# Kernel tuning notes

Measured on AMD Instinct MI355X. Metric: run time of the kernel, lower is better.

Reference implementation:

```python
import jax, jax.numpy as jnp
import numpy as np

DIM = 192
NUM_HEADS = 6
HEAD_DIM = DIM // NUM_HEADS
SCALE = HEAD_DIM ** -0.5


def setup_inputs() -> dict:
    key = jax.random.key(0)
    ks = jax.random.split(key, 4)
    B_, N, C = 4096, 64, DIM  # num_windows*B, Wh*Ww, dim
    nW = 64
    w_std = 0.02  # trunc-normal-ish init scale to keep logits sane
    x = jax.random.normal(ks[0], (B_, N, C), dtype=jnp.float32)
    mask = jnp.zeros((nW, N, N), dtype=jnp.float32)  # 0/-inf shift mask; zeros here
    qkv_w = jax.random.normal(ks[1], (3 * C, C), dtype=jnp.float32) * w_std
    qkv_b = jnp.zeros((3 * C,), dtype=jnp.float32)
    proj_w = jax.random.normal(ks[2], (C, C), dtype=jnp.float32) * w_std
    proj_b = jnp.zeros((C,), dtype=jnp.float32)
    return {"x": x, "mask": mask, "qkv_w": qkv_w, "qkv_b": qkv_b,
            "proj_w": proj_w, "proj_b": proj_b}


def reference(x, mask, qkv_w, qkv_b, proj_w, proj_b):
    B_, N, C = x.shape
    H, hd = NUM_HEADS, HEAD_DIM
    # qkv projection: torch Linear is x @ W.T + b
    qkv = x @ qkv_w.T + qkv_b                       # [B_, N, 3C]
    qkv = qkv.reshape(B_, N, 3, H, hd)
    qkv = jnp.transpose(qkv, (2, 0, 3, 1, 4))       # [3, B_, H, N, hd]
    q, k, v = qkv[0], qkv[1], qkv[2]
    attn = jnp.einsum('bhnd,bhmd->bhnm', q * SCALE, k)  # [B_, H, N, N]
    nW = mask.shape[0]
    attn = attn.reshape(B_ // nW, nW, H, N, N) + mask[None, :, None, :, :]
    attn = jax.nn.softmax(attn.reshape(B_, H, N, N), axis=-1)
    out = jnp.einsum('bhnm,bhmd->bnhd', attn, v).reshape(B_, N, C)
    out = out @ proj_w.T + proj_b
    return out
```

## Files before the change

kernel.cpp:

```cpp
#include <hip/hip_runtime.h>
#include <stdint.h>
#include <stddef.h>

#define NWIN   64
#define NTOK   64
#define CDIM   192
#define NHEAD  6
#define HDIM   32
constexpr float SCALE = 0.17677669529663687f;

typedef float   f32x4  __attribute__((ext_vector_type(4)));
typedef float   fvec4  __attribute__((ext_vector_type(4)));
typedef __bf16  bfx8   __attribute__((ext_vector_type(8)));
typedef __bf16  bfx4   __attribute__((ext_vector_type(4)));

static __device__ __forceinline__ bfx8 pack8(fvec4 a, fvec4 b) {
  bfx8 r;
  r[0] = (__bf16)a[0]; r[1] = (__bf16)a[1]; r[2] = (__bf16)a[2]; r[3] = (__bf16)a[3];
  r[4] = (__bf16)b[0]; r[5] = (__bf16)b[1]; r[6] = (__bf16)b[2]; r[7] = (__bf16)b[3];
  return r;
}

#define LDS_BYTES 130048

__global__ void __launch_bounds__(512, 1)
wattn_fused(const float* __restrict__ x, const float* __restrict__ mask,
            const float* __restrict__ qkv_w, const float* __restrict__ qkv_b,
            const float* __restrict__ proj_w, const float* __restrict__ proj_b,
            float* __restrict__ out)
{
  extern __shared__ char smem[];
  __bf16* qk = (__bf16*)(smem);
  __bf16* vT = (__bf16*)(smem + 50176);
  float*  pf = (float*)(smem + 77824);
  __bf16* pb = (__bf16*)(smem + 95232);
  __bf16* xb = (__bf16*)(smem + 104448);
  __bf16* ao = xb;

  const int b    = blockIdx.x;
  const int tid  = threadIdx.x;
  const int wv   = tid >> 6;
  const int lane = tid & 63;
  const int r16  = lane & 15;
  const int q4   = lane >> 4;

  {
    const float* xg = x + (size_t)b * (NTOK * CDIM);
#pragma unroll
    for (int it = 0; it < 6; ++it) {
      int i   = tid + it * 512;
      int row = i / 48;
      int col = (i % 48) * 4;
      fvec4 v = *(const fvec4*)(xg + i * 4);
      bfx4 p; p[0] = (__bf16)v[0]; p[1] = (__bf16)v[1];
              p[2] = (__bf16)v[2]; p[3] = (__bf16)v[3];
      *(bfx4*)(xb + row * 200 + col) = p;
    }
  }
  __syncthreads();

  {
    f32x4 acc[5][4];
#pragma unroll
    for (int cl = 0; cl < 5; ++cl)
#pragma unroll
      for (int rt = 0; rt < 4; ++rt) acc[cl][rt] = (f32x4){0.f, 0.f, 0.f, 0.f};

    for (int k = 0; k < 6; ++k) {
      bfx8 af[4];
#pragma unroll
      for (int rt = 0; rt < 4; ++rt)
        af[rt] = *(const bfx8*)(xb + (rt * 16 + r16) * 200 + k * 32 + q4 * 8);
#pragma unroll
      for (int cl = 0; cl < 5; ++cl) {
        int ct = wv + cl * 8;
        if (ct < 36) {
          const float* wp = qkv_w + (size_t)(ct * 16 + r16) * 192 + k * 32 + q4 * 8;
          bfx8 bf = pack8(*(const fvec4*)wp, *(const fvec4*)(wp + 4));
#pragma unroll
          for (int rt = 0; rt < 4; ++rt)
            acc[cl][rt] = __builtin_amdgcn_mfma_f32_16x16x32_bf16(
                af[rt], bf, acc[cl][rt], 0, 0, 0);
        }
      }
    }
#pragma unroll
    for (int cl = 0; cl < 5; ++cl) {
      int ct = wv + cl * 8;
      if (ct < 36) {
        float bias = qkv_b[ct * 16 + r16];
        if (ct < 24) {
#pragma unroll
          for (int rt = 0; rt < 4; ++rt) {
#pragma unroll
            for (int r = 0; r < 4; ++r)
              qk[(rt * 16 + q4 * 4 + r) * 392 + ct * 16 + r16] =
                  (__bf16)(acc[cl][rt][r] + bias);
          }
        } else {
          int h = (ct - 24) >> 1;
          int d = ((ct - 24) & 1) * 16 + r16;
#pragma unroll
          for (int rt = 0; rt < 4; ++rt) {
            bfx4 p;
#pragma unroll
            for (int r = 0; r < 4; ++r) p[r] = (__bf16)(acc[cl][rt][r] + bias);
            *(bfx4*)(vT + (h * 32 + d) * 72 + rt * 16 + q4 * 4) = p;
          }
        }
      }
    }
  }
  __syncthreads();

  const int wmask = b & (NWIN - 1);
  for (int h = 0; h < 6; ++h) {
    {
      int nt = wv >> 1;
      bfx8 qf = *(const bfx8*)(qk + (nt * 16 + r16) * 392 + h * 32 + q4 * 8);
      f32x4 z = (f32x4){0.f, 0.f, 0.f, 0.f};
#pragma unroll
      for (int j = 0; j < 2; ++j) {
        int mt = (wv & 1) * 2 + j;
        bfx8 kf = *(const bfx8*)(qk + (mt * 16 + r16) * 392 + 192 + h * 32 + q4 * 8);
        f32x4 s = __builtin_amdgcn_mfma_f32_16x16x32_bf16(qf, kf, z, 0, 0, 0);
#pragma unroll
        for (int r = 0; r < 4; ++r)
          pf[(nt * 16 + q4 * 4 + r) * 68 + mt * 16 + r16] = s[r];
      }
    }
    __syncthreads();
    {
      int n  = tid >> 3;
      int s8 = (tid & 7) * 8;
      const float* mrow = mask + ((size_t)wmask * 64 + n) * 64 + s8;
      fvec4 m0 = *(const fvec4*)(mrow);
      fvec4 m1 = *(const fvec4*)(mrow + 4);
      float v[8];
#pragma unroll
      for (int i = 0; i < 4; ++i) v[i]     = pf[n * 68 + s8 + i]     * SCALE + m0[i];
#pragma unroll
      for (int i = 0; i < 4; ++i) v[4 + i] = pf[n * 68 + s8 + 4 + i] * SCALE + m1[i];
      float mx = v[0];
#pragma unroll
      for (int i = 1; i < 8; ++i) mx = fmaxf(mx, v[i]);
      mx = fmaxf(mx, __shfl_xor(mx, 1));
      mx = fmaxf(mx, __shfl_xor(mx, 2));
      mx = fmaxf(mx, __shfl_xor(mx, 4));
      float sum = 0.f;
#pragma unroll
      for (int i = 0; i < 8; ++i) { v[i] = __expf(v[i] - mx); sum += v[i]; }
      sum += __shfl_xor(sum, 1);
      sum += __shfl_xor(sum, 2);
      sum += __shfl_xor(sum, 4);
      float inv = 1.f / sum;
      bfx8 p;
#pragma unroll
      for (int i = 0; i < 8; ++i) p[i] = (__bf16)(v[i] * inv);
      *(bfx8*)(pb + n * 72 + s8) = p;
    }
    __syncthreads();
    {
      int nt = wv >> 1, dt = wv & 1;
      f32x4 acc = (f32x4){0.f, 0.f, 0.f, 0.f};
#pragma unroll
      for (int kk = 0; kk < 2; ++kk) {
        bfx8 pa = *(const bfx8*)(pb + (nt * 16 + r16) * 72 + kk * 32 + q4 * 8);
        bfx8 vb = *(const bfx8*)(vT + (h * 32 + dt * 16 + r16) * 72 + kk * 32 + q4 * 8);
        acc = __builtin_amdgcn_mfma_f32_16x16x32_bf16(pa, vb, acc, 0, 0, 0);
      }
#pragma unroll
      for (int r = 0; r < 4; ++r)
        ao[(nt * 16 + q4 * 4 + r) * 200 + h * 32 + dt * 16 + r16] = (__bf16)acc[r];
    }
    __syncthreads();
  }

  {
    f32x4 acc[3][2];
#pragma unroll
    for (int u = 0; u < 3; ++u)
#pragma unroll
      for (int j = 0; j < 2; ++j) acc[u][j] = (f32x4){0.f, 0.f, 0.f, 0.f};

    for (int k = 0; k < 6; ++k) {
#pragma unroll
      for (int u = 0; u < 3; ++u) {
        int uid  = wv + u * 8;
        int ct   = uid % 12;
        int half = uid / 12;
        const float* wp = proj_w + (size_t)(ct * 16 + r16) * 192 + k * 32 + q4 * 8;
        bfx8 bf = pack8(*(const fvec4*)wp, *(const fvec4*)(wp + 4));
#pragma unroll
        for (int j = 0; j < 2; ++j) {
          int rt = half * 2 + j;
          bfx8 af = *(const bfx8*)(ao + (rt * 16 + r16) * 200 + k * 32 + q4 * 8);
          acc[u][j] = __builtin_amdgcn_mfma_f32_16x16x32_bf16(af, bf, acc[u][j], 0, 0, 0);
        }
      }
    }
    float* og = out + (size_t)b * (NTOK * CDIM);
#pragma unroll
    for (int u = 0; u < 3; ++u) {
      int uid  = wv + u * 8;
      int ct   = uid % 12;
      int half = uid / 12;
      float bias = proj_b[ct * 16 + r16];
#pragma unroll
      for (int j = 0; j < 2; ++j) {
        int rt = half * 2 + j;
#pragma unroll
        for (int r = 0; r < 4; ++r)
          og[(rt * 16 + q4 * 4 + r) * 192 + ct * 16 + r16] = acc[u][j][r] + bias;
      }
    }
  }
}

extern "C" void kernel_launch(void* const* d_in, const int* in_sizes, int n_in,
                              void* d_out, int out_size, void* d_ws, size_t ws_size,
                              hipStream_t stream) {
  (void)in_sizes; (void)n_in; (void)d_ws; (void)ws_size; (void)out_size;
  const float* x      = (const float*)d_in[0];
  const float* mask   = (const float*)d_in[1];
  const float* qkv_w  = (const float*)d_in[2];
  const float* qkv_b  = (const float*)d_in[3];
  const float* proj_w = (const float*)d_in[4];
  const float* proj_b = (const float*)d_in[5];
  float* out = (float*)d_out;

  hipFuncSetAttribute((const void*)wattn_fused,
                      hipFuncAttributeMaxDynamicSharedMemorySize, LDS_BYTES);
  wattn_fused<<<dim3(4096), dim3(512), LDS_BYTES, stream>>>(
      x, mask, qkv_w, qkv_b, proj_w, proj_b, out);
}
```

Before: 750.0 us.

## Keep softmax in registers, drop LDS staging of x, raise block occupancy

The attention phase now computes S transposed (K as the A operand) so each lane holds a full softmax row slice. Max and sum are reduced with cross-lane shuffles, and the bf16 probabilities are shuffled into A-operand layout for the PV MFMA. This removes the fp32 score and probability LDS buffers and the per-head barriers. The QKV projection reads x straight from global memory into bf16 fragments, with each wave doing 18 column tiles for one row tile. LDS drops from 130048 to 77824 bytes and launch bounds allow more blocks per CU, at the cost of more register pressure and redundant global reads of x.

```diff
diff --git a/kernel.cpp b/kernel.cpp
--- a/kernel.cpp
+++ b/kernel.cpp
@@ -5,37 +5,39 @@
 #define NWIN   64
 #define NTOK   64
 #define CDIM   192
-#define NHEAD  6
-#define HDIM   32
 constexpr float SCALE = 0.17677669529663687f;
 
-typedef float   f32x4  __attribute__((ext_vector_type(4)));
-typedef float   fvec4  __attribute__((ext_vector_type(4)));
-typedef __bf16  bfx8   __attribute__((ext_vector_type(8)));
-typedef __bf16  bfx4   __attribute__((ext_vector_type(4)));
-
-static __device__ __forceinline__ bfx8 pack8(fvec4 a, fvec4 b) {
+typedef float    f32x4 __attribute__((ext_vector_type(4)));
+typedef __bf16   bfx8  __attribute__((ext_vector_type(8)));
+typedef __bf16   bfx4  __attribute__((ext_vector_type(4)));
+typedef uint32_t u32;
+
+union PAu { u32 w[4]; bfx8 v; };
+
+static __device__ __forceinline__ bfx8 pack8(f32x4 a, f32x4 b) {
   bfx8 r;
   r[0] = (__bf16)a[0]; r[1] = (__bf16)a[1]; r[2] = (__bf16)a[2]; r[3] = (__bf16)a[3];
   r[4] = (__bf16)b[0]; r[5] = (__bf16)b[1]; r[6] = (__bf16)b[2]; r[7] = (__bf16)b[3];
   return r;
 }
-
-#define LDS_BYTES 130048
-
-__global__ void __launch_bounds__(512, 1)
+static __device__ __forceinline__ u32 pk2(float a, float b) {
+  union { __bf16 h[2]; u32 w; } t;
+  t.h[0] = (__bf16)a; t.h[1] = (__bf16)b;
+  return t.w;
+}
+
+#define LDS_BYTES 77824
+
+__global__ void __launch_bounds__(512, 4)
 wattn_fused(const float* __restrict__ x, const float* __restrict__ mask,
             const float* __restrict__ qkv_w, const float* __restrict__ qkv_b,
             const float* __restrict__ proj_w, const float* __restrict__ proj_b,
             float* __restrict__ out)
 {
   extern __shared__ char smem[];
-  __bf16* qk = (__bf16*)(smem);
+  __bf16* qk = (__bf16*)smem;
   __bf16* vT = (__bf16*)(smem + 50176);
-  float*  pf = (float*)(smem + 77824);
-  __bf16* pb = (__bf16*)(smem + 95232);
-  __bf16* xb = (__bf16*)(smem + 104448);
-  __bf16* ao = xb;
+  __bf16* ao = (__bf16*)smem;
 
   const int b    = blockIdx.x;
   const int tid  = threadIdx.x;
@@ -44,174 +46,165 @@
   const int r16  = lane & 15;
   const int q4   = lane >> 4;
 
+  const float* xg = x + (size_t)b * (NTOK * CDIM);
+
   {
-    const float* xg = x + (size_t)b * (NTOK * CDIM);
-#pragma unroll
-    for (int it = 0; it < 6; ++it) {
-      int i   = tid + it * 512;
-      int row = i / 48;
-      int col = (i % 48) * 4;
-      fvec4 v = *(const fvec4*)(xg + i * 4);
-      bfx4 p; p[0] = (__bf16)v[0]; p[1] = (__bf16)v[1];
-              p[2] = (__bf16)v[2]; p[3] = (__bf16)v[3];
-      *(bfx4*)(xb + row * 200 + col) = p;
+    const int rt = wv & 3;
+    const int c0 = (wv >> 2) * 18;
+    f32x4 acc[18];
+#pragma unroll
+    for (int i = 0; i < 18; ++i) acc[i] = (f32x4){0.f, 0.f, 0.f, 0.f};
+
+    for (int k = 0; k < 6; ++k) {
+      const float* ap = xg + (rt * 16 + r16) * 192 + k * 32 + q4 * 8;
+      bfx8 af = pack8(*(const f32x4*)ap, *(const f32x4*)(ap + 4));
+#pragma unroll
+      for (int i = 0; i < 18; ++i) {
+        const float* wp = qkv_w + (size_t)((c0 + i) * 16 + r16) * 192 + k * 32 + q4 * 8;
+        bfx8 bf = pack8(*(const f32x4*)wp, *(const f32x4*)(wp + 4));
+        acc[i] = __builtin_amdgcn_mfma_f32_16x16x32_bf16(af, bf, acc[i], 0, 0, 0);
+      }
+    }
+#pragma unroll
+    for (int i = 0; i < 18; ++i) {
+      const int ct = c0 + i;
+      const float bias = qkv_b[ct * 16 + r16];
+      if (ct < 24) {
+#pragma unroll
+        for (int r = 0; r < 4; ++r)
+          qk[(rt * 16 + q4 * 4 + r) * 392 + ct * 16 + r16] =
+              (__bf16)(acc[i][r] + bias);
+      } else {
+        const int hh = (ct - 24) >> 1;
+        const int d  = ((ct - 24) & 1) * 16 + r16;
+        bfx4 p;
+#pragma unroll
+        for (int r = 0; r < 4; ++r) p[r] = (__bf16)(acc[i][r] + bias);
+        *(bfx4*)(vT + (hh * 32 + d) * 72 + rt * 16 + q4 * 4) = p;
+      }
     }
   }
   __syncthreads();
 
-  {
-    f32x4 acc[5][4];
-#pragma unroll
-    for (int cl = 0; cl < 5; ++cl)
-#pragma unroll
-      for (int rt = 0; rt < 4; ++rt) acc[cl][rt] = (f32x4){0.f, 0.f, 0.f, 0.f};
-
-    for (int k = 0; k < 6; ++k) {
-      bfx8 af[4];
-#pragma unroll
-      for (int rt = 0; rt < 4; ++rt)
-        af[rt] = *(const bfx8*)(xb + (rt * 16 + r16) * 200 + k * 32 + q4 * 8);
-#pragma unroll
-      for (int cl = 0; cl < 5; ++cl) {
-        int ct = wv + cl * 8;
-        if (ct < 36) {
-          const float* wp = qkv_w + (size_t)(ct * 16 + r16) * 192 + k * 32 + q4 * 8;
-          bfx8 bf = pack8(*(const fvec4*)wp, *(const fvec4*)(wp + 4));
-#pragma unroll
-          for (int rt = 0; rt < 4; ++rt)
-            acc[cl][rt] = __builtin_amdgcn_mfma_f32_16x16x32_bf16(
-                af[rt], bf, acc[cl][rt], 0, 0, 0);
-        }
-      }
-    }
-#pragma unroll
-    for (int cl = 0; cl < 5; ++cl) {
-      int ct = wv + cl * 8;
-      if (ct < 36) {
-        float bias = qkv_b[ct * 16 + r16];
-        if (ct < 24) {
-#pragma unroll
-          for (int rt = 0; rt < 4; ++rt) {
-#pragma unroll
-            for (int r = 0; r < 4; ++r)
-              qk[(rt * 16 + q4 * 4 + r) * 392 + ct * 16 + r16] =
-                  (__bf16)(acc[cl][rt][r] + bias);
-          }
-        } else {
-          int h = (ct - 24) >> 1;
-          int d = ((ct - 24) & 1) * 16 + r16;
-#pragma unroll
-          for (int rt = 0; rt < 4; ++rt) {
-            bfx4 p;
-#pragma unroll
-            for (int r = 0; r < 4; ++r) p[r] = (__bf16)(acc[cl][rt][r] + bias);
-            *(bfx4*)(vT + (h * 32 + d) * 72 + rt * 16 + q4 * 4) = p;
-          }
-        }
+  const int wmask = b & (NWIN - 1);
+  const int nt = wv & 3;
+  const int h0 = wv >> 2;
+  const int srcA = r16 + ((lane & 16) << 1);
+  const int srcB = srcA + 16;
+  const bool hiT = (lane & 32) != 0;
+  f32x4 o[3][2];
+#pragma unroll
+  for (int hp = 0; hp < 3; ++hp)
+#pragma unroll
+    for (int dt = 0; dt < 2; ++dt) o[hp][dt] = (f32x4){0.f, 0.f, 0.f, 0.f};
+
+#pragma unroll
+  for (int hp = 0; hp < 3; ++hp) {
+    const int h = 2 * hp + h0;
+    bfx8 qb = *(const bfx8*)(qk + (nt * 16 + r16) * 392 + h * 32 + q4 * 8);
+    f32x4 st[4];
+#pragma unroll
+    for (int mt = 0; mt < 4; ++mt) {
+      bfx8 ka = *(const bfx8*)(qk + (mt * 16 + r16) * 392 + 192 + h * 32 + q4 * 8);
+      st[mt] = __builtin_amdgcn_mfma_f32_16x16x32_bf16(
+          ka, qb, (f32x4){0.f, 0.f, 0.f, 0.f}, 0, 0, 0);
+    }
+    float lg[16];
+    const float* mrow = mask + ((size_t)wmask * 64 + nt * 16 + r16) * 64 + q4 * 4;
+#pragma unroll
+    for (int mt = 0; mt < 4; ++mt) {
+      f32x4 mk = *(const f32x4*)(mrow + mt * 16);
+#pragma unroll
+      for (int r = 0; r < 4; ++r) lg[mt * 4 + r] = st[mt][r] * SCALE + mk[r];
+    }
+    float mx = lg[0];
+#pragma unroll
+    for (int i2 = 1; i2 < 16; ++i2) mx = fmaxf(mx, lg[i2]);
+    mx = fmaxf(mx, __shfl_xor(mx, 16));
+    mx = fmaxf(mx, __shfl_xor(mx, 32));
+    float sum = 0.f;
+#pragma unroll
+    for (int i2 = 0; i2 < 16; ++i2) { lg[i2] = __expf(lg[i2] - mx); sum += lg[i2]; }
+    sum += __shfl_xor(sum, 16);
+    sum += __shfl_xor(sum, 32);
+    const float inv = 1.f / sum;
+    u32 u[4][2];
+#pragma unroll
+    for (int mt = 0; mt < 4; ++mt) {
+      u[mt][0] = pk2(lg[mt * 4 + 0] * inv, lg[mt * 4 + 1] * inv);
+      u[mt][1] = pk2(lg[mt * 4 + 2] * inv, lg[mt * 4 + 3] * inv);
+    }
+#pragma unroll
+    for (int kk = 0; kk < 2; ++kk) {
+      const int a0l = __shfl((int)u[kk * 2][0],     srcA, 64);
+      const int a1l = __shfl((int)u[kk * 2][1],     srcA, 64);
+      const int a0h = __shfl((int)u[kk * 2 + 1][0], srcA, 64);
+      const int a1h = __shfl((int)u[kk * 2 + 1][1], srcA, 64);
+      const int b0l = __shfl((int)u[kk * 2][0],     srcB, 64);
+      const int b1l = __shfl((int)u[kk * 2][1],     srcB, 64);
+      const int b0h = __shfl((int)u[kk * 2 + 1][0], srcB, 64);
+      const int b1h = __shfl((int)u[kk * 2 + 1][1], srcB, 64);
+      PAu pa;
+      pa.w[0] = (u32)(hiT ? a0h : a0l);
+      pa.w[1] = (u32)(hiT ? a1h : a1l);
+      pa.w[2] = (u32)(hiT ? b0h : b0l);
+      pa.w[3] = (u32)(hiT ? b1h : b1l);
+#pragma unroll
+      for (int dt = 0; dt < 2; ++dt) {
+        bfx8 vb = *(const bfx8*)(vT + (h * 32 + dt * 16 + r16) * 72 + kk * 32 + q4 * 8);
+        o[hp][dt] = __builtin_amdgcn_mfma_f32_16x16x32_bf16(pa.v, vb, o[hp][dt], 0, 0, 0);
       }
     }
   }
   __syncthreads();
-
-  const int wmask = b & (NWIN - 1);
-  for (int h = 0; h < 6; ++h) {
-    {
-      int nt = wv >> 1;
-      bfx8 qf = *(const bfx8*)(qk + (nt * 16 + r16) * 392 + h * 32 + q4 * 8);
-      f32x4 z = (f32x4){0.f, 0.f, 0.f, 0.f};
-#pragma unroll
-      for (int j = 0; j < 2; ++j) {
-        int mt = (wv & 1) * 2 + j;
-        bfx8 kf = *(const bfx8*)(qk + (mt * 16 + r16) * 392 + 192 + h * 32 + q4 * 8);
-        f32x4 s = __builtin_amdgcn_mfma_f32_16x16x32_bf16(qf, kf, z, 0, 0, 0);
-#pragma unroll
-        for (int r = 0; r < 4; ++r)
-          pf[(nt * 16 + q4 * 4 + r) * 68 + mt * 16 + r16] = s[r];
-      }
-    }
-    __syncthreads();
-    {
-      int n  = tid >> 3;
-      int s8 = (tid & 7) * 8;
-      const float* mrow = mask + ((size_t)wmask * 64 + n) * 64 + s8;
-      fvec4 m0 = *(const fvec4*)(mrow);
-      fvec4 m1 = *(const fvec4*)(mrow + 4);
-      float v[8];
-#pragma unroll
-      for (int i = 0; i < 4; ++i) v[i]     = pf[n * 68 + s8 + i]     * SCALE + m0[i];
-#pragma unroll
-      for (int i = 0; i < 4; ++i) v[4 + i] = pf[n * 68 + s8 + 4 + i] * SCALE + m1[i];
-      float mx = v[0];
-#pragma unroll
-      for (int i = 1; i < 8; ++i) mx = fmaxf(mx, v[i]);
-      mx = fmaxf(mx, __shfl_xor(mx, 1));
-      mx = fmaxf(mx, __shfl_xor(mx, 2));
-      mx = fmaxf(mx, __shfl_xor(mx, 4));
-      float sum = 0.f;
-#pragma unroll
-      for (int i = 0; i < 8; ++i) { v[i] = __expf(v[i] - mx); sum += v[i]; }
-      sum += __shfl_xor(sum, 1);
-      sum += __shfl_xor(sum, 2);
-      sum += __shfl_xor(sum, 4);
-      float inv = 1.f / sum;
-      bfx8 p;
-#pragma unroll
-      for (int i = 0; i < 8; ++i) p[i] = (__bf16)(v[i] * inv);
-      *(bfx8*)(pb + n * 72 + s8) = p;
-    }
-    __syncthreads();
-    {
-      int nt = wv >> 1, dt = wv & 1;
-      f32x4 acc = (f32x4){0.f, 0.f, 0.f, 0.f};
-#pragma unroll
-      for (int kk = 0; kk < 2; ++kk) {
-        bfx8 pa = *(const bfx8*)(pb + (nt * 16 + r16) * 72 + kk * 32 + q4 * 8);
-        bfx8 vb = *(const bfx8*)(vT + (h * 32 + dt * 16 + r16) * 72 + kk * 32 + q4 * 8);
-        acc = __builtin_amdgcn_mfma_f32_16x16x32_bf16(pa, vb, acc, 0, 0, 0);
-      }
+#pragma unroll
+  for (int hp = 0; hp < 3; ++hp) {
+    const int h = 2 * hp + h0;
+#pragma unroll
+    for (int dt = 0; dt < 2; ++dt)
 #pragma unroll
       for (int r = 0; r < 4; ++r)
-        ao[(nt * 16 + q4 * 4 + r) * 200 + h * 32 + dt * 16 + r16] = (__bf16)acc[r];
-    }
-    __syncthreads();
-  }
+        ao[(nt * 16 + q4 * 4 + r) * 200 + h * 32 + dt * 16 + r16] =
+            (__bf16)o[hp][dt][r];
+  }
+  __syncthreads();
 
   {
     f32x4 acc[3][2];
 #pragma unroll
-    for (int u = 0; u < 3; ++u)
-#pragma unroll
-      for (int j = 0; j < 2; ++j) acc[u][j] = (f32x4){0.f, 0.f, 0.f, 0.f};
+    for (int u2 = 0; u2 < 3; ++u2)
+#pragma unroll
+      for (int j = 0; j < 2; ++j) acc[u2][j] = (f32x4){0.f, 0.f, 0.f, 0.f};
 
     for (int k = 0; k < 6; ++k) {
 #pragma unroll
-      for (int u = 0; u < 3; ++u) {
-        int uid  = wv + u * 8;
-        int ct   = uid % 12;
-        int half = uid / 12;
+      for (int u2 = 0; u2 < 3; ++u2) {
+        const int uid  = wv + u2 * 8;
+        const int ct   = uid % 12;
+        const int half = uid / 12;
         const float* wp = proj_w + (size_t)(ct * 16 + r16) * 192 + k * 32 + q4 * 8;
-        bfx8 bf = pack8(*(const fvec4*)wp, *(const fvec4*)(wp + 4));
+        bfx8 bf = pack8(*(const f32x4*)wp, *(const f32x4*)(wp + 4));
 #pragma unroll
         for (int j = 0; j < 2; ++j) {
-          int rt = half * 2 + j;
+          const int rt = half * 2 + j;
           bfx8 af = *(const bfx8*)(ao + (rt * 16 + r16) * 200 + k * 32 + q4 * 8);
-          acc[u][j] = __builtin_amdgcn_mfma_f32_16x16x32_bf16(af, bf, acc[u][j], 0, 0, 0);
+          acc[u2][j] = __builtin_amdgcn_mfma_f32_16x16x32_bf16(af, bf, acc[u2][j], 0, 0, 0);
         }
       }
     }
     float* og = out + (size_t)b * (NTOK * CDIM);
 #pragma unroll
-    for (int u = 0; u < 3; ++u) {
-      int uid  = wv + u * 8;
-      int ct   = uid % 12;
-      int half = uid / 12;
-      float bias = proj_b[ct * 16 + r16];
+    for (int u2 = 0; u2 < 3; ++u2) {
+      const int uid  = wv + u2 * 8;
+      const int ct   = uid % 12;
+      const int half = uid / 12;
+      const float bias = proj_b[ct * 16 + r16];
 #pragma unroll
       for (int j = 0; j < 2; ++j) {
-        int rt = half * 2 + j;
+        const int rt = half * 2 + j;
 #pragma unroll
         for (int r = 0; r < 4; ++r)
-          og[(rt * 16 + q4 * 4 + r) * 192 + ct * 16 + r16] = acc[u][j][r] + bias;
+          og[(rt * 16 + q4 * 4 + r) * 192 + ct * 16 + r16] = acc[u2][j][r] + bias;
       }
     }
   }
```

Result: slower. 1.224 ms (+63.1%).
